# Performance work log

Hardware: AMD Instinct MI355X
Metric: run time of the kernel (lower is better)

Reference implementation:

```python
import jax, jax.numpy as jnp
import numpy as np

N = 64          # num_nodes (EEG electrodes)
T = 200         # time steps
B = 64          # batch
H = 64          # hidden_dim
K = 3           # cheb_k
F_IN = 1        # input_dim
D_GRU = 2 * H * N  # 8192, GRU input size


def setup_inputs() -> dict:
    key = jax.random.key(0)
    ks = jax.random.split(key, 24)
    s = 0.05
    inp = {
        "x": jax.random.normal(ks[0], (B, N, T), dtype=jnp.float32),
        "spatial_ei": jax.random.randint(ks[1], (2, 512), 0, N, dtype=jnp.int32),
        "spatial_ew": jax.random.uniform(ks[2], (512,), dtype=jnp.float32),
        "functional_ei": jax.random.randint(ks[3], (2, 1024), 0, N, dtype=jnp.int32),
        "functional_ew": jax.random.uniform(ks[4], (1024,), dtype=jnp.float32),
        # ChebConv: K separate Linear(F_IN->H, bias shared once)
        "Wcheb": jax.random.normal(ks[5], (K, F_IN, H), dtype=jnp.float32) * s,
        "bcheb": jnp.zeros((H,), jnp.float32),
        # GCNConv
        "Wgcn": jax.random.normal(ks[6], (F_IN, H), dtype=jnp.float32) * s,
        "bgcn": jnp.zeros((H,), jnp.float32),
        # bidirectional GRU (torch layout: gates r,z,n stacked -> 3H rows)
        "Wih_f": jax.random.normal(ks[7], (3 * H, D_GRU), dtype=jnp.float32) * s,
        "Whh_f": jax.random.normal(ks[8], (3 * H, H), dtype=jnp.float32) * s,
        "bih_f": jnp.zeros((3 * H,), jnp.float32),
        "bhh_f": jnp.zeros((3 * H,), jnp.float32),
        "Wih_b": jax.random.normal(ks[9], (3 * H, D_GRU), dtype=jnp.float32) * s,
        "Whh_b": jax.random.normal(ks[10], (3 * H, H), dtype=jnp.float32) * s,
        "bih_b": jnp.zeros((3 * H,), jnp.float32),
        "bhh_b": jnp.zeros((3 * H,), jnp.float32),
        # attention + classifier heads
        "attn_W": jax.random.normal(ks[11], (2 * H, 1), dtype=jnp.float32) * s,
        "attn_b": jnp.zeros((1,), jnp.float32),
        "clf_W": jax.random.normal(ks[12], (2 * H, 1), dtype=jnp.float32) * s,
        "clf_b": jnp.zeros((1,), jnp.float32),
    }
    return inp


def _gru_scan(xp, Whh, bhh, reverse):
    # xp: [B, T, 3H] precomputed input projection; returns [B, T, H]
    xp_t = jnp.swapaxes(xp, 0, 1)  # [T, B, 3H]
    Hh = Whh.shape[1]

    def step(h, xg):
        hg = h @ Whh.T + bhh
        xr, xz, xn = jnp.split(xg, 3, axis=-1)
        hr, hz, hn = jnp.split(hg, 3, axis=-1)
        r = jax.nn.sigmoid(xr + hr)
        z = jax.nn.sigmoid(xz + hz)
        n = jnp.tanh(xn + r * hn)
        h_new = (1.0 - z) * n + z * h
        return h_new, h_new

    h0 = jnp.zeros((xp.shape[0], Hh), xp.dtype)
    _, hs = jax.lax.scan(step, h0, xp_t, reverse=reverse)
    return jnp.swapaxes(hs, 0, 1)


def _forward(x, spatial_ei, spatial_ew, functional_ei, functional_ew,
             Wcheb, bcheb, Wgcn, bgcn,
             Wih_f, Whh_f, bih_f, bhh_f, Wih_b, Whh_b, bih_b, bhh_b,
             attn_W, attn_b, clf_W, clf_b):
    x = x[..., None]  # [B, N, T, 1] (the x.dim()==3 -> unsqueeze path)
    Bsz, Nn, Tt, _ = x.shape

    # ---- ChebConv (PyG, sym norm, lambda_max=2): L_tilde = -D^-1/2 A D^-1/2
    # (scaled-Laplacian self loops cancel: 2*1/2 - 1 = 0)
    row, col = spatial_ei[0], spatial_ei[1]
    deg = jax.ops.segment_sum(spatial_ew, row, num_segments=Nn)
    dinv = jnp.where(deg > 0, jax.lax.rsqrt(jnp.where(deg > 0, deg, 1.0)), 0.0)
    wn = dinv[row] * spatial_ew * dinv[col]
    # operator S[i, j]: aggregate source j into target i (source_to_target flow)
    S = jnp.zeros((Nn, Nn), x.dtype).at[col, row].add(wn)
    Ltil = -S
    Tx0 = x
    Tx1 = jnp.einsum('ij,bjtf->bitf', Ltil, Tx0)
    out_s = jnp.einsum('bntf,fh->bnth', Tx0, Wcheb[0]) + jnp.einsum('bntf,fh->bnth', Tx1, Wcheb[1])
    for k in range(2, K):
        Tx2 = 2.0 * jnp.einsum('ij,bjtf->bitf', Ltil, Tx1) - Tx0
        out_s = out_s + jnp.einsum('bntf,fh->bnth', Tx2, Wcheb[k])
        Tx0, Tx1 = Tx1, Tx2
    h_sp = out_s + bcheb  # [B, N, T, H]

    # ---- GCNConv (PyG gcn_norm with self loops, weight 1)
    row, col = functional_ei[0], functional_ei[1]
    deg = jax.ops.segment_sum(functional_ew, col, num_segments=Nn) + 1.0
    dinv = jax.lax.rsqrt(deg)
    wn = dinv[row] * functional_ew * dinv[col]
    Sg = jnp.zeros((Nn, Nn), x.dtype).at[col, row].add(wn) + jnp.diag(dinv * dinv)
    h_fn = jnp.einsum('bntf,fh->bnth', jnp.einsum('ij,bjtf->bitf', Sg, x), Wgcn) + bgcn

    # ---- stack over time, flatten nodes
    h = jnp.concatenate([h_sp, h_fn], axis=-1)           # [B, N, T, 2H]
    gru_in = jnp.transpose(h, (0, 2, 1, 3)).reshape(Bsz, Tt, Nn * 2 * H)

    # ---- bidirectional GRU
    xp_f = jnp.einsum('btd,gd->btg', gru_in, Wih_f) + bih_f
    xp_b = jnp.einsum('btd,gd->btg', gru_in, Wih_b) + bih_b
    h_f = _gru_scan(xp_f, Whh_f, bhh_f, reverse=False)
    h_b = _gru_scan(xp_b, Whh_b, bhh_b, reverse=True)
    gru_out = jnp.concatenate([h_f, h_b], axis=-1)       # [B, T, 2H]

    # ---- attention pooling + classifier
    scores = jnp.tanh(gru_out @ attn_W + attn_b)         # [B, T, 1]
    aw = jax.nn.softmax(scores, axis=1)
    ctx = jnp.sum(aw * gru_out, axis=1)                  # [B, 2H]
    return jax.nn.sigmoid(ctx @ clf_W + clf_b)           # [B, 1]


def reference(x, spatial_ei, spatial_ew, functional_ei, functional_ew,
              Wcheb, bcheb, Wgcn, bgcn,
              Wih_f, Whh_f, bih_f, bhh_f, Wih_b, Whh_b, bih_b, bhh_b,
              attn_W, attn_b, clf_W, clf_b):
    return _forward(x, spatial_ei, spatial_ew, functional_ei, functional_ew,
                    Wcheb, bcheb, Wgcn, bgcn,
                    Wih_f, Whh_f, bih_f, bhh_f, Wih_b, Whh_b, bih_b, bhh_b,
                    attn_W, attn_b, clf_W, clf_b)
```

## Files before the change

kernel.cpp:

```cpp
#include <hip/hip_runtime.h>
#include <math.h>

#define Nn 64
#define Tt 200
#define Bb 64

__device__ __forceinline__ float sigm(float x){ return 1.0f/(1.0f+__expf(-x)); }
__device__ __forceinline__ float tanh_fast(float x){
  x = fminf(fmaxf(x, -15.f), 15.f);
  float e = __expf(-2.f*x);
  return (1.f - e)/(1.f + e);
}

typedef __attribute__((ext_vector_type(2))) _Float16 h2v;
typedef __attribute__((ext_vector_type(4))) float f4;

#if __has_builtin(__builtin_amdgcn_fdot2)
#define DOT2(w,hv,acc) __builtin_amdgcn_fdot2((w),(hv),(acc),false)
#else
#define DOT2(w,hv,acc) fmaf((float)(w)[0],(float)(hv)[0], fmaf((float)(w)[1],(float)(hv)[1],(acc)))
#endif

__global__ __launch_bounds__(256) void k1_graphs(
    const int* __restrict__ sp_ei, const float* __restrict__ sp_ew,
    const int* __restrict__ fn_ei, const float* __restrict__ fn_ew,
    float* __restrict__ Lg, float* __restrict__ L2g, float* __restrict__ Gm)
{
  __shared__ float deg[Nn];
  __shared__ float dinv[Nn];
  __shared__ float S[64*68];
  const int tid = threadIdx.x;

  if (tid < Nn) deg[tid] = 0.f;
  for (int i=tid;i<64*68;i+=256) S[i]=0.f;
  __syncthreads();
  for (int e=tid;e<512;e+=256) atomicAdd(&deg[sp_ei[e]], sp_ew[e]);
  __syncthreads();
  if (tid < Nn) dinv[tid] = (deg[tid] > 0.f) ? rsqrtf(deg[tid]) : 0.f;
  __syncthreads();
  for (int e=tid;e<512;e+=256) {
    int r = sp_ei[e], c = sp_ei[512+e];
    atomicAdd(&S[c*68 + r], dinv[r]*sp_ew[e]*dinv[c]);
  }
  __syncthreads();
  for (int i=tid;i<4096;i+=256) Lg[i] = -S[(i>>6)*68 + (i&63)];
  {
    const int n = tid>>2, mb = (tid&3)*16;
    float a[16];
    #pragma unroll
    for (int q=0;q<16;q++) a[q]=0.f;
    for (int j=0;j<64;j++){
      float snj = S[n*68+j];
      const float4* rj = (const float4*)&S[j*68+mb];
      #pragma unroll
      for (int q=0;q<4;q++){
        float4 v = rj[q];
        a[q*4+0]=fmaf(snj,v.x,a[q*4+0]);
        a[q*4+1]=fmaf(snj,v.y,a[q*4+1]);
        a[q*4+2]=fmaf(snj,v.z,a[q*4+2]);
        a[q*4+3]=fmaf(snj,v.w,a[q*4+3]);
      }
    }
    #pragma unroll
    for (int q=0;q<16;q++){
      int m = mb+q;
      L2g[n*64+m] = 2.f*a[q] - (n==m ? 1.f : 0.f);
    }
  }
  __syncthreads();

  if (tid < Nn) deg[tid] = 0.f;
  for (int i=tid;i<64*68;i+=256) S[i]=0.f;
  __syncthreads();
  for (int e=tid;e<1024;e+=256) atomicAdd(&deg[fn_ei[1024+e]], fn_ew[e]);
  __syncthreads();
  if (tid < Nn) dinv[tid] = rsqrtf(deg[tid] + 1.f);
  __syncthreads();
  for (int e=tid;e<1024;e+=256) {
    int r = fn_ei[e], c = fn_ei[1024+e];
    atomicAdd(&S[c*68 + r], dinv[r]*fn_ew[e]*dinv[c]);
  }
  __syncthreads();
  if (tid < Nn) S[tid*68 + tid] += dinv[tid]*dinv[tid];
  __syncthreads();
  for (int i=tid;i<4096;i+=256) Gm[i] = S[(i>>6)*68 + (i&63)];
}

__global__ __launch_bounds__(64) void k2_aeff(
    const float* __restrict__ Wih_f, const float* __restrict__ bih_f,
    const float* __restrict__ Wih_b, const float* __restrict__ bih_b,
    const float* __restrict__ Wcheb, const float* __restrict__ bcheb,
    const float* __restrict__ Wgcn,  const float* __restrict__ bgcn,
    const float* __restrict__ Lg, const float* __restrict__ L2g,
    const float* __restrict__ Gm,
    float* __restrict__ Aeff, float* __restrict__ constv)
{
  const int g = blockIdx.x;
  const int dir = (g >= 192) ? 1 : 0;
  const int grow = dir ? g - 192 : g;
  const float* Wih = dir ? Wih_b : Wih_f;
  const float* bih = dir ? bih_b : bih_f;

  __shared__ float wrow[64*129];
  __shared__ float arow[256];
  const int tid = threadIdx.x;

  for (int i = tid; i < 8192; i += 64)
    wrow[(i>>7)*129 + (i&127)] = Wih[grow*8192 + i];
  __syncthreads();

  const int n = tid;
  float a0=0.f,a1=0.f,a2=0.f,a3=0.f,cp=0.f;
  for (int c=0;c<64;c++) {
    float w1 = wrow[n*129 + c];
    a0 = fmaf(w1, Wcheb[c],     a0);
    a1 = fmaf(w1, Wcheb[64+c],  a1);
    a2 = fmaf(w1, Wcheb[128+c], a2);
    cp = fmaf(w1, bcheb[c],     cp);
    float w2 = wrow[n*129 + 64 + c];
    a3 = fmaf(w2, Wgcn[c], a3);
    cp = fmaf(w2, bgcn[c], cp);
  }
  arow[n*4+0]=a0; arow[n*4+1]=a1; arow[n*4+2]=a2; arow[n*4+3]=a3;
  for (int off=32; off; off>>=1) cp += __shfl_down(cp, off, 64);
  if (tid==0) constv[g] = cp + bih[grow];
  __syncthreads();

  const int m = tid;
  float ae = arow[m*4+0];
  for (int nn2=0; nn2<64; nn2++) {
    ae = fmaf(arow[nn2*4+1], Lg [nn2*64+m], ae);
    ae = fmaf(arow[nn2*4+2], L2g[nn2*64+m], ae);
    ae = fmaf(arow[nn2*4+3], Gm [nn2*64+m], ae);
  }
  Aeff[g*64+m] = ae;
}

__global__ __launch_bounds__(256) void k3_transpose(
    const float* __restrict__ x, float* __restrict__ xTr)
{
  const int b = blockIdx.x;
  for (int idx = threadIdx.x; idx < Tt*Nn; idx += 256) {
    int t = idx >> 6, m = idx & 63;
    xTr[(b*Tt + t)*64 + m] = x[(b*64 + m)*Tt + t];
  }
}

__global__ __launch_bounds__(256) void k4_gemm(
    const float* __restrict__ xTr, const float* __restrict__ Aeff,
    const float* __restrict__ constv, float* __restrict__ xp)
{
  const int m0 = blockIdx.x*64, g0 = blockIdx.y*64;
  __shared__ float sX[64*68];
  __shared__ float sA[64*68];
  const int tid = threadIdx.x;
  const float4* xTr4 = (const float4*)xTr;
  const float4* A4   = (const float4*)Aeff;

  #pragma unroll
  for (int i=0;i<4;i++) {
    int f = tid + i*256;
    int row = f >> 4, kq = f & 15;
    float4 v = xTr4[(m0+row)*16 + kq];
    float vv[4] = {v.x,v.y,v.z,v.w};
    float4 w = A4[(g0+row)*16 + kq];
    float wv[4] = {w.x,w.y,w.z,w.w};
    #pragma unroll
    for (int q=0;q<4;q++) {
      sX[(kq*4+q)*68 + row] = vv[q];
      sA[(kq*4+q)*68 + row] = wv[q];
    }
  }
  __syncthreads();

  const int tm = tid & 15, tn = tid >> 4;
  float acc[4][4] = {};
  #pragma unroll 8
  for (int k=0;k<64;k++) {
    float4 a  = *(const float4*)&sX[k*68 + tm*4];
    float4 bb = *(const float4*)&sA[k*68 + tn*4];
    float av[4]={a.x,a.y,a.z,a.w}, bv[4]={bb.x,bb.y,bb.z,bb.w};
    #pragma unroll
    for (int i=0;i<4;i++)
      #pragma unroll
      for (int j=0;j<4;j++)
        acc[i][j] = fmaf(av[i], bv[j], acc[i][j]);
  }

  float cv[4];
  #pragma unroll
  for (int j=0;j<4;j++) cv[j] = constv[g0 + tn*4 + j];
  #pragma unroll
  for (int i=0;i<4;i++) {
    int mrow = m0 + tm*4 + i;
    #pragma unroll
    for (int j=0;j<4;j++)
      xp[mrow*384 + g0 + tn*4 + j] = acc[i][j] + cv[j];
  }
}

__global__ __launch_bounds__(64)
__attribute__((amdgpu_waves_per_eu(1, 1)))
void k5_gru(
    const float* __restrict__ xp,
    const float* __restrict__ Whh_f, const float* __restrict__ bhh_f,
    const float* __restrict__ Whh_b, const float* __restrict__ bhh_b,
    float* __restrict__ gru_out)
{
  const int bd = blockIdx.x;
  const int b = bd >> 1, dir = bd & 1;
  const int g = threadIdx.x & 63;
  const float* Whh = dir ? Whh_b : Whh_f;
  const float* bhh = dir ? bhh_b : bhh_f;

  h2v wr[32], wz[32], wn[32];
  #pragma unroll
  for (int i=0;i<32;i++){
    float2 a = ((const float2*)(Whh + (size_t)g*64))[i];
    float2 bq= ((const float2*)(Whh + (size_t)(64+g)*64))[i];
    float2 c = ((const float2*)(Whh + (size_t)(128+g)*64))[i];
    wr[i] = h2v{(_Float16)a.x, (_Float16)a.y};
    wz[i] = h2v{(_Float16)bq.x,(_Float16)bq.y};
    wn[i] = h2v{(_Float16)c.x, (_Float16)c.y};
  }
  const float br_ = bhh[g], bz_ = bhh[64+g], bn_ = bhh[128+g];

  __shared__ __align__(16) _Float16 hsh[64];
  hsh[g] = (_Float16)0.f;

  const int t0 = dir ? (Tt-1) : 0;
  const int tstep = dir ? -1 : 1;
  const float* xb = xp + (size_t)(b*Tt)*384 + dir*192 + g;
  float* gout = gru_out + (size_t)(b*Tt)*128 + dir*64 + g;

  float h = 0.f;
  float xrA = xb[(size_t)t0*384], xzA = xb[(size_t)t0*384+64], xnA = xb[(size_t)t0*384+128];
  const int t1 = t0 + tstep;
  float xrB = xb[(size_t)t1*384], xzB = xb[(size_t)t1*384+64], xnB = xb[(size_t)t1*384+128];

  int t = t0;
  auto STEP = [&](float& xr, float& xz, float& xn){
    h2v hv[32];
    {
      const uint4* hp4 = (const uint4*)hsh;
      #pragma unroll
      for (int q=0;q<8;q++){
        union { uint4 v; h2v p[4]; } uu;
        uu.v = hp4[q];
        hv[q*4+0]=uu.p[0]; hv[q*4+1]=uu.p[1]; hv[q*4+2]=uu.p[2]; hv[q*4+3]=uu.p[3];
      }
    }

    const float cxr = xr, cxz = xz, cxn = xn;
    const int tpre = t + 2*tstep;
    if ((unsigned)tpre < (unsigned)Tt) {
      xr = xb[(size_t)tpre*384];
      xz = xb[(size_t)tpre*384+64];
      xn = xb[(size_t)tpre*384+128];
    }

    float ar0=0.f,ar1=0.f,az0=0.f,az1=0.f,an0=0.f,an1=0.f;
    #pragma unroll
    for (int i=0;i<32;i+=2){
      ar0 = DOT2(wr[i],  hv[i],  ar0);  az0 = DOT2(wz[i],  hv[i],  az0);  an0 = DOT2(wn[i],  hv[i],  an0);
      ar1 = DOT2(wr[i+1],hv[i+1],ar1);  az1 = DOT2(wz[i+1],hv[i+1],az1);  an1 = DOT2(wn[i+1],hv[i+1],an1);
    }

    float r   = sigm(cxr + (ar0+ar1) + br_);
    float z   = sigm(cxz + (az0+az1) + bz_);
    float nn2 = tanh_fast(cxn + r*((an0+an1) + bn_));
    float hnew = (1.f - z)*nn2 + z*h;
    h = hnew;
    hsh[g] = (_Float16)hnew;
    gout[(size_t)t*128] = hnew;
    t += tstep;
  };

  for (int sp=0; sp<Tt; sp+=2) { STEP(xrA,xzA,xnA); STEP(xrB,xzB,xnB); }
}

__global__ __launch_bounds__(256) void k6_attn(
    const float* __restrict__ gru_out,
    const float* __restrict__ attn_W, const float* __restrict__ attn_b,
    const float* __restrict__ clf_W,  const float* __restrict__ clf_b,
    float* __restrict__ out)
{
  const int b = blockIdx.x, tid = threadIdx.x;
  __shared__ float s_s[Tt];
  __shared__ float red[256];
  __shared__ float aW[128], cW[128];
  if (tid < 128) { aW[tid]=attn_W[tid]; cW[tid]=clf_W[tid]; }
  __syncthreads();

  if (tid < Tt) {
    const float* row = gru_out + (b*Tt + tid)*128;
    float acc = 0.f;
    for (int j=0;j<128;j++) acc = fmaf(row[j], aW[j], acc);
    s_s[tid] = tanhf(acc + attn_b[0]);
  }
  __syncthreads();

  red[tid] = (tid < Tt) ? s_s[tid] : -1e30f;
  __syncthreads();
  for (int s2=128;s2;s2>>=1){ if(tid<s2) red[tid]=fmaxf(red[tid],red[tid+s2]); __syncthreads(); }
  float mx = red[0];
  __syncthreads();

  float e = 0.f;
  if (tid < Tt) { e = expf(s_s[tid]-mx); s_s[tid] = e; }
  red[tid] = e;
  __syncthreads();
  for (int s2=128;s2;s2>>=1){ if(tid<s2) red[tid]+=red[tid+s2]; __syncthreads(); }
  float total = red[0];
  __syncthreads();

  float p = 0.f;
  if (tid < 128) {
    float c = 0.f;
    for (int t=0;t<Tt;t++) c = fmaf(s_s[t], gru_out[(b*Tt+t)*128 + tid], c);
    p = (c/total)*cW[tid];
  }
  red[tid] = p;
  __syncthreads();
  for (int s2=128;s2;s2>>=1){ if(tid<s2) red[tid]+=red[tid+s2]; __syncthreads(); }
  if (tid==0) out[b] = sigm(red[0] + clf_b[0]);
}

extern "C" void kernel_launch(void* const* d_in, const int* in_sizes, int n_in,
                              void* d_out, int out_size, void* d_ws, size_t ws_size,
                              hipStream_t stream)
{
  const float* x      = (const float*)d_in[0];
  const int*   sp_ei  = (const int*)  d_in[1];
  const float* sp_ew  = (const float*)d_in[2];
  const int*   fn_ei  = (const int*)  d_in[3];
  const float* fn_ew  = (const float*)d_in[4];
  const float* Wcheb  = (const float*)d_in[5];
  const float* bcheb  = (const float*)d_in[6];
  const float* Wgcn   = (const float*)d_in[7];
  const float* bgcn   = (const float*)d_in[8];
  const float* Wih_f  = (const float*)d_in[9];
  const float* Whh_f  = (const float*)d_in[10];
  const float* bih_f  = (const float*)d_in[11];
  const float* bhh_f  = (const float*)d_in[12];
  const float* Wih_b  = (const float*)d_in[13];
  const float* Whh_b  = (const float*)d_in[14];
  const float* bih_b  = (const float*)d_in[15];
  const float* bhh_b  = (const float*)d_in[16];
  const float* attn_W = (const float*)d_in[17];
  const float* attn_b = (const float*)d_in[18];
  const float* clf_W  = (const float*)d_in[19];
  const float* clf_b  = (const float*)d_in[20];
  float* out = (float*)d_out;

  float* ws     = (float*)d_ws;
  float* Lg     = ws;
  float* L2g    = Lg   + 4096;
  float* Gm     = L2g  + 4096;
  float* Aeff   = Gm   + 4096;
  float* constv = Aeff + 24576;
  float* xTr    = constv + 512;
  float* xp     = xTr  + 819200;
  float* gro    = xp   + 4915200;

  hipLaunchKernelGGL(k1_graphs,    dim3(1),      dim3(256), 0, stream,
                     sp_ei, sp_ew, fn_ei, fn_ew, Lg, L2g, Gm);
  hipLaunchKernelGGL(k3_transpose, dim3(64),     dim3(256), 0, stream, x, xTr);
  hipLaunchKernelGGL(k2_aeff,      dim3(384),    dim3(64),  0, stream,
                     Wih_f, bih_f, Wih_b, bih_b, Wcheb, bcheb, Wgcn, bgcn,
                     Lg, L2g, Gm, Aeff, constv);
  hipLaunchKernelGGL(k4_gemm,      dim3(200, 6), dim3(256), 0, stream,
                     xTr, Aeff, constv, xp);
  hipLaunchKernelGGL(k5_gru,       dim3(128),    dim3(64),  0, stream,
                     xp, Whh_f, bhh_f, Whh_b, bhh_b, gro);
  hipLaunchKernelGGL(k6_attn,      dim3(64),     dim3(256), 0, stream,
                     gro, attn_W, attn_b, clf_W, clf_b, out);
}
```

Baseline: 145.3 us.

## Fuse input transpose into GEMM load and interleave GRU LDS reads with dots

Drops the separate transpose kernel. The GEMM now reads x directly in its strided native layout while filling the shared-memory tile, which removes one launch and a full round trip of the transposed buffer. The GRU step also loads the half-precision hidden state from LDS in chunks and places those loads between the dot-product groups using sched_group_barrier, so LDS latency overlaps with compute on the serial critical path. The risk is that the direct x loads are strided by the time dimension, so their coalescing may be worse than before.

```diff
diff --git a/kernel.cpp b/kernel.cpp
--- a/kernel.cpp
+++ b/kernel.cpp
@@ -136,39 +136,39 @@
   Aeff[g*64+m] = ae;
 }
 
-__global__ __launch_bounds__(256) void k3_transpose(
-    const float* __restrict__ x, float* __restrict__ xTr)
-{
-  const int b = blockIdx.x;
-  for (int idx = threadIdx.x; idx < Tt*Nn; idx += 256) {
-    int t = idx >> 6, m = idx & 63;
-    xTr[(b*Tt + t)*64 + m] = x[(b*64 + m)*Tt + t];
-  }
-}
-
 __global__ __launch_bounds__(256) void k4_gemm(
-    const float* __restrict__ xTr, const float* __restrict__ Aeff,
+    const float* __restrict__ x, const float* __restrict__ Aeff,
     const float* __restrict__ constv, float* __restrict__ xp)
 {
   const int m0 = blockIdx.x*64, g0 = blockIdx.y*64;
   __shared__ float sX[64*68];
   __shared__ float sA[64*68];
   const int tid = threadIdx.x;
-  const float4* xTr4 = (const float4*)xTr;
-  const float4* A4   = (const float4*)Aeff;
-
-  #pragma unroll
-  for (int i=0;i<4;i++) {
-    int f = tid + i*256;
-    int row = f >> 4, kq = f & 15;
-    float4 v = xTr4[(m0+row)*16 + kq];
-    float vv[4] = {v.x,v.y,v.z,v.w};
-    float4 w = A4[(g0+row)*16 + kq];
-    float wv[4] = {w.x,w.y,w.z,w.w};
-    #pragma unroll
-    for (int q=0;q<4;q++) {
-      sX[(kq*4+q)*68 + row] = vv[q];
-      sA[(kq*4+q)*68 + row] = wv[q];
+
+  {
+    const int row = tid & 63;
+    const int kq  = tid >> 6;
+    const int m = m0 + row;
+    const int b = m / 200;
+    const int t = m - b*200;
+    const float* xb = x + (size_t)b*64*200 + t;
+    #pragma unroll
+    for (int kk=0; kk<16; ++kk) {
+      int k = kq*16 + kk;
+      sX[k*68 + row] = xb[(size_t)k*200];
+    }
+  }
+  {
+    const float4* A4 = (const float4*)Aeff;
+    #pragma unroll
+    for (int i=0;i<4;i++) {
+      int f = tid + i*256;
+      int r2 = f >> 4, kq2 = f & 15;
+      float4 w = A4[(g0+r2)*16 + kq2];
+      sA[(kq2*4+0)*68 + r2] = w.x;
+      sA[(kq2*4+1)*68 + r2] = w.y;
+      sA[(kq2*4+2)*68 + r2] = w.z;
+      sA[(kq2*4+3)*68 + r2] = w.w;
     }
   }
   __syncthreads();
@@ -240,17 +240,6 @@
 
   int t = t0;
   auto STEP = [&](float& xr, float& xz, float& xn){
-    h2v hv[32];
-    {
-      const uint4* hp4 = (const uint4*)hsh;
-      #pragma unroll
-      for (int q=0;q<8;q++){
-        union { uint4 v; h2v p[4]; } uu;
-        uu.v = hp4[q];
-        hv[q*4+0]=uu.p[0]; hv[q*4+1]=uu.p[1]; hv[q*4+2]=uu.p[2]; hv[q*4+3]=uu.p[3];
-      }
-    }
-
     const float cxr = xr, cxz = xz, cxn = xn;
     const int tpre = t + 2*tstep;
     if ((unsigned)tpre < (unsigned)Tt) {
@@ -259,12 +248,37 @@
       xn = xb[(size_t)tpre*384+128];
     }
 
+    const uint4* hp4 = (const uint4*)hsh;
+    union U { uint4 v; h2v p[4]; };
     float ar0=0.f,ar1=0.f,az0=0.f,az1=0.f,an0=0.f,an1=0.f;
-    #pragma unroll
-    for (int i=0;i<32;i+=2){
-      ar0 = DOT2(wr[i],  hv[i],  ar0);  az0 = DOT2(wz[i],  hv[i],  az0);  an0 = DOT2(wn[i],  hv[i],  an0);
-      ar1 = DOT2(wr[i+1],hv[i+1],ar1);  az1 = DOT2(wz[i+1],hv[i+1],az1);  an1 = DOT2(wn[i+1],hv[i+1],an1);
-    }
+
+#define DOTS8(U0,U1,base)                                                     \
+    { _Pragma("unroll")                                                       \
+      for (int j=0;j<4;j++){                                                  \
+        ar0=DOT2(wr[(base)+j],  U0.p[j],ar0);                                 \
+        az0=DOT2(wz[(base)+j],  U0.p[j],az0);                                 \
+        an0=DOT2(wn[(base)+j],  U0.p[j],an0);                                 \
+        ar1=DOT2(wr[(base)+4+j],U1.p[j],ar1);                                 \
+        az1=DOT2(wz[(base)+4+j],U1.p[j],az1);                                 \
+        an1=DOT2(wn[(base)+4+j],U1.p[j],an1);                                 \
+      } }
+
+    U A0,A1,B0,B1,C0,C1,D0,D1;
+    A0.v=hp4[0]; A1.v=hp4[1]; B0.v=hp4[2]; B1.v=hp4[3];
+    __builtin_amdgcn_sched_group_barrier(0x100, 4, 0);
+    DOTS8(A0,A1,0);
+    __builtin_amdgcn_sched_group_barrier(0x2, 24, 0);
+    C0.v=hp4[4]; C1.v=hp4[5];
+    __builtin_amdgcn_sched_group_barrier(0x100, 2, 0);
+    DOTS8(B0,B1,8);
+    __builtin_amdgcn_sched_group_barrier(0x2, 24, 0);
+    D0.v=hp4[6]; D1.v=hp4[7];
+    __builtin_amdgcn_sched_group_barrier(0x100, 2, 0);
+    DOTS8(C0,C1,16);
+    __builtin_amdgcn_sched_group_barrier(0x2, 24, 0);
+    DOTS8(D0,D1,24);
+    __builtin_amdgcn_sched_group_barrier(0x2, 24, 0);
+#undef DOTS8
 
     float r   = sigm(cxr + (ar0+ar1) + br_);
     float z   = sigm(cxz + (az0+az1) + bz_);
@@ -359,18 +373,16 @@
   float* Gm     = L2g  + 4096;
   float* Aeff   = Gm   + 4096;
   float* constv = Aeff + 24576;
-  float* xTr    = constv + 512;
-  float* xp     = xTr  + 819200;
+  float* xp     = constv + 512;
   float* gro    = xp   + 4915200;
 
   hipLaunchKernelGGL(k1_graphs,    dim3(1),      dim3(256), 0, stream,
                      sp_ei, sp_ew, fn_ei, fn_ew, Lg, L2g, Gm);
-  hipLaunchKernelGGL(k3_transpose, dim3(64),     dim3(256), 0, stream, x, xTr);
   hipLaunchKernelGGL(k2_aeff,      dim3(384),    dim3(64),  0, stream,
                      Wih_f, bih_f, Wih_b, bih_b, Wcheb, bcheb, Wgcn, bgcn,
                      Lg, L2g, Gm, Aeff, constv);
   hipLaunchKernelGGL(k4_gemm,      dim3(200, 6), dim3(256), 0, stream,
-                     xTr, Aeff, constv, xp);
+                     x, Aeff, constv, xp);
   hipLaunchKernelGGL(k5_gru,       dim3(128),    dim3(64),  0, stream,
                      xp, Whh_f, bhh_f, Whh_b, bhh_b, gro);
   hipLaunchKernelGGL(k6_attn,      dim3(64),     dim3(256), 0, stream,
```

Measured after the change: 136.9 us. 5.8% less time.
